# Optimization experiments

Hardware: AMD Instinct MI355X
Metric: run time of the kernel (lower is better)

Reference implementation:

```python
import jax, jax.numpy as jnp
import numpy as np

NEG = -9.0e15
EPS = 1e-5  # torch BatchNorm1d default eps


def _chain_idx(n):
    # chain graph with self loops; row-major nonzero ordering (matches torch .nonzero())
    rows, cols = [], []
    for i in range(n):
        for j in (i - 1, i, i + 1):
            if 0 <= j < n:
                rows.append(i); cols.append(j)
    return np.asarray(rows, np.int32), np.asarray(cols, np.int32)


def semgconv(x, W, e, rows, cols, n, b):
    # x: [B,N,Fin]; W: [2,Fin,Fout]; e: [nnz]; returns [B,N,Fout]
    h0 = jnp.einsum('bnf,fo->bno', x, W[0])
    h1 = jnp.einsum('bnf,fo->bno', x, W[1])
    logits = jnp.full((n, n), NEG, x.dtype).at[rows, cols].set(e)
    A = jax.nn.softmax(logits, axis=1)              # row-wise softmax over masked adjacency
    d = jnp.diagonal(A)                             # adj * I contribution
    A_off = A - jnp.diag(d)                         # adj * (1 - I)
    out = d[None, :, None] * h0 + jnp.einsum('ij,bjf->bif', A_off, h1)
    return out + b


def gblock(x, W, e, rows, cols, n, b, g, be):
    # SemGraphConv -> BatchNorm1d (training-mode batch stats over (B,N)) -> ReLU
    h = semgconv(x, W, e, rows, cols, n, b)
    mu = h.mean(axis=(0, 1))
    var = h.var(axis=(0, 1))
    h = g * (h - mu) * jax.lax.rsqrt(var + EPS) + be
    return jax.nn.relu(h)


def setup_inputs() -> dict:
    key = jax.random.key(0)
    ks = iter(jax.random.split(key, 40))
    B, NC, NS, H, HS = 4096, 32, 10, 160, 512  # HS = int(160/10*32)
    rc, cc = _chain_idx(NC)
    rs, cs = _chain_idx(NS)
    nnz_c, nnz_s = len(rc), len(rs)

    def w(shape, scale=0.1):
        return jax.random.normal(next(ks), shape, jnp.float32) * scale

    return dict(
        x_c=jax.random.normal(next(ks), (B, NC, 2), jnp.float32),
        x_s=jax.random.normal(next(ks), (B, NS, 2), jnp.float32),
        W_in=w((2, 2, H)), e_in=w((nnz_c,)) + 1.0, b_in=w((H,)),
        g_in=jnp.ones((H,), jnp.float32), be_in=jnp.zeros((H,), jnp.float32),
        W_s1=w((2, 2, HS)), e_s1=w((nnz_s,)) + 1.0, b_s1=w((HS,)),
        g_s1=jnp.ones((HS,), jnp.float32), be_s1=jnp.zeros((HS,), jnp.float32),
        W_c320=w((3, 2, 2 * H, H)), e_c320=w((3, nnz_c)) + 1.0, b_c320=w((3, H)),
        g_c320=jnp.ones((3, H), jnp.float32), be_c320=jnp.zeros((3, H), jnp.float32),
        W_c160=w((6, 2, H, H)), e_c160=w((6, nnz_c)) + 1.0, b_c160=w((6, H)),
        g_c160=jnp.ones((6, H), jnp.float32), be_c160=jnp.zeros((6, H), jnp.float32),
        W_s512=w((2, 2, HS, HS)), e_s512=w((2, nnz_s)) + 1.0, b_s512=w((2, HS)),
        g_s512=jnp.ones((2, HS), jnp.float32), be_s512=jnp.zeros((2, HS), jnp.float32),
        W_out=w((2, H, 2)), e_out=w((nnz_c,)) + 1.0, b_out=w((2,)),
        mc_r=jnp.asarray(rc), mc_c=jnp.asarray(cc),
        ms_r=jnp.asarray(rs), ms_c=jnp.asarray(cs),
    )


def reference(x_c, x_s, W_in, e_in, b_in, g_in, be_in,
              W_s1, e_s1, b_s1, g_s1, be_s1,
              W_c320, e_c320, b_c320, g_c320, be_c320,
              W_c160, e_c160, b_c160, g_c160, be_c160,
              W_s512, e_s512, b_s512, g_s512, be_s512,
              W_out, e_out, b_out, mc_r, mc_c, ms_r, ms_c):
    B, NC, NS, H = x_c.shape[0], 32, 10, 160
    c = gblock(x_c, W_in, e_in, mc_r, mc_c, NC, b_in, g_in, be_in)
    s = gblock(x_s, W_s1, e_s1, ms_r, ms_c, NS, b_s1, g_s1, be_s1)   # [B,10,512]
    for i in range(3):  # c_block1..3 interleaved with s_block2..3
        s_r = jnp.transpose(s, (0, 2, 1)).reshape(B, NC, H)          # [B,512,10] -> [B,32,160]
        c = gblock(jnp.concatenate([c, s_r], axis=2),
                   W_c320[i], e_c320[i], mc_r, mc_c, NC,
                   b_c320[i], g_c320[i], be_c320[i])
        h = gblock(c, W_c160[2 * i], e_c160[2 * i], mc_r, mc_c, NC,
                   b_c160[2 * i], g_c160[2 * i], be_c160[2 * i])
        h = gblock(h, W_c160[2 * i + 1], e_c160[2 * i + 1], mc_r, mc_c, NC,
                   b_c160[2 * i + 1], g_c160[2 * i + 1], be_c160[2 * i + 1])
        c = c + h                                                     # _ResGraphConv residual
        if i < 2:
            s = gblock(s, W_s512[i], e_s512[i], ms_r, ms_c, NS,
                       b_s512[i], g_s512[i], be_s512[i])
    return jax.nn.sigmoid(semgconv(c, W_out, e_out, mc_r, mc_c, NC, b_out))
```

## Files before the change

### kernel.cpp

```cpp
#include <hip/hip_runtime.h>
#include <hip/hip_bf16.h>

typedef __hip_bfloat16 bf16;
typedef unsigned short u16;
typedef __attribute__((ext_vector_type(8))) short short8;
typedef __attribute__((ext_vector_type(8))) unsigned short u16x8;
typedef __attribute__((ext_vector_type(4))) float f32x4;

#define B_SZ  4096
#define NCN   32
#define NSN   10
#define MC    (B_SZ*NCN)
#define MS    (B_SZ*NSN)
#define BUF_ELEMS 20971520UL

#define MODE_IN  0
#define MODE_PL  1
#define MODE_CC  2

#define DT_BF16  0
#define DT_F32   1
#define DT_PROBE 2

#define PART_SLOTS 163840
#define W_TOTAL    3411968

__device__ __forceinline__ float bf2f(bf16 v) { return __bfloat162float(v); }
__device__ __forceinline__ float ldv(const void* p, int dt, int idx) {
    return dt ? ((const float*)p)[idx] : bf2f(((const bf16*)p)[idx]);
}
__device__ __forceinline__ int resolve(int dt, const u16* probe) {
    return (dt == DT_PROBE) ? ((probe[0] == 0x3F80u) ? DT_BF16 : DT_F32) : dt;
}
__device__ __forceinline__ u16 f2bfbits(float f) {
    unsigned u = __builtin_bit_cast(unsigned, f);
    u += 0x7FFFu + ((u >> 16) & 1u);
    return (u16)(u >> 16);
}
__device__ __forceinline__ float bits2f(u16 u) {
    return __builtin_bit_cast(float, (unsigned)u << 16);
}
__device__ __forceinline__ void gload_lds16(const u16* g, u16* l) {
    __builtin_amdgcn_global_load_lds(
        (const __attribute__((address_space(1))) void*)g,
        (__attribute__((address_space(3))) void*)l, 16, 0, 0);
}
__device__ __forceinline__ size_t cfrag_addr(int r, int k) {
    int RT = r >> 8, within = r & 255;
    int g = ((within >> 6) << 2) | ((within >> 4) & 3);
    int tg = k >> 5, q = (k >> 3) & 3, j = k & 7;
    return ((((size_t)RT * 5 + tg) * 16 + g) * 64 + q * 16 + (r & 15)) * 8 + j;
}

struct WD { const void* src; int srcOff; int dstOff; int K; int F; };
struct WArgs { WD d[13]; };

__global__ void presplit_kernel(WArgs a, const u16* __restrict__ probe,
                                u16* __restrict__ Wf) {
    WD D = a.d[blockIdx.y];
    int nsteps = (D.K + 31) / 32;
    int total = (D.F / 32) * nsteps * 4096;
    int idx = blockIdx.x * blockDim.x + threadIdx.x;
    if (idx >= total) return;
    int dt = resolve(DT_PROBE, probe);
    int per = nsteps * 4096;
    int chunk = idx / per;  int rem = idx - chunk * per;
    int s = rem >> 12;      int slot = rem & 4095;
    int half = slot >> 11;  int sl = slot & 2047;
    int nt = sl >> 9;       int within = sl & 511;
    int lane = within >> 3; int j = within & 7;
    int q = lane >> 4, l15 = lane & 15;
    int plane = nt >> 1;
    int fcol = chunk * 32 + (nt & 1) * 16 + l15;
    int k = s * 32 + q * 8 + j;
    float v = (k < D.K) ? ldv(D.src, dt, D.srcOff + plane * D.K * D.F + k * D.F + fcol) : 0.f;
    u16 hb = f2bfbits(v);
    Wf[D.dstOff + idx] = half ? f2bfbits(v - bits2f(hb)) : hb;
}

struct CD { const void* e; int off; int n; };
struct CArgs { CD d[14]; };

__global__ void coeffs_all(CArgs a, const u16* __restrict__ probe, float* __restrict__ cfb) {
    CD D = a.d[blockIdx.x];
    float* cf = cfb + blockIdx.x * 96;
    int dt = resolve(DT_PROBE, probe);
    int i = threadIdx.x;
    if (i >= D.n) return;
    bool hasL = (i > 0), hasR = (i < D.n - 1);
    int off = D.off + ((i == 0) ? 0 : (3 * i - 1));
    float el = hasL ? ldv(D.e, dt, off) : 0.f;
    float es = ldv(D.e, dt, off + (hasL ? 1 : 0));
    float er = hasR ? ldv(D.e, dt, off + (hasL ? 2 : 1)) : 0.f;
    float m = es;
    if (hasL) m = fmaxf(m, el);
    if (hasR) m = fmaxf(m, er);
    float xl = hasL ? expf(el - m) : 0.f;
    float xs = expf(es - m);
    float xr = hasR ? expf(er - m) : 0.f;
    float inv = 1.f / (xl + xs + xr);
    cf[i]           = xl * inv;
    cf[D.n + i]     = xs * inv;
    cf[2 * D.n + i] = xr * inv;
}

template<int WAVES, int NODES, int KT, int TMODE, int AFRAG>
__global__ __launch_bounds__(WAVES * 64, (WAVES == 4) ? 4 : 3) void gemm_mfma(
    const u16* __restrict__ Wf, int wtOff,
    const u16* __restrict__ aHi, const u16* __restrict__ bHi2,
    const void* __restrict__ raw,
    const void* __restrict__ bias, int bOff,
    const u16* __restrict__ probe, const float* __restrict__ cf,
    u16* __restrict__ Thi,
    float* __restrict__ sumP, float* __restrict__ sqP, int F)
{
    constexpr int THREADS = WAVES * 64;
    constexpr int ROWS   = WAVES * 64;
    constexpr int nsteps = (KT + 31) / 32;
    constexpr int CHUNK  = (nsteps % 5 == 0) ? 5 : ((nsteps % 4 == 0) ? 4 : 1);
    constexpr int NCHUNK = nsteps / CHUNK;
    constexpr int NGRP   = WAVES * 4;
    constexpr int W_BYTES   = CHUNK * 8192;
    constexpr int VL_BYTES  = ROWS * 36 * 4;
    constexpr int RED_ONE   = 32 * (WAVES * 4) * 4;
    constexpr int EPI_BYTES = VL_BYTES + 2 * RED_ONE;
    constexpr int SMEM_SZ   = (W_BYTES > EPI_BYTES) ? W_BYTES : EPI_BYTES;

    const int tid  = threadIdx.x;
    const int wave = tid >> 6, lane = tid & 63;
    const int l15  = lane & 15, q = lane >> 4;

    const int NY   = F >> 5;
    const int nwg  = gridDim.x;
    const int NX   = nwg / NY;
    const int orig = blockIdx.x;
    const int xcd  = orig & 7, pos = orig >> 3;
    const int qch  = nwg >> 3, rch = nwg & 7;
    const int lin  = (xcd < rch ? xcd * (qch + 1)
                                : rch * (qch + 1) + (xcd - rch) * qch) + pos;
    const int bx   = lin / NY;
    const int by   = lin - bx * NY;
    const int f0   = by * 32;
    const int row0 = bx * ROWS;
    const int wdt  = resolve(DT_PROBE, probe);

    __shared__ __align__(16) char smem[SMEM_SZ];
    u16* Wt = (u16*)smem;
    float (*Vl)[36] = (float(*)[36])smem;
    float (*redS)[WAVES * 4] = (float(*)[WAVES * 4])(smem + VL_BYTES);
    float (*redQ)[WAVES * 4] = (float(*)[WAVES * 4])(smem + VL_BYTES + RED_ONE);

    const u16* wbase = Wf + wtOff + (size_t)by * nsteps * 4096;

    f32x4 acc[4][4];
#pragma unroll
    for (int a = 0; a < 4; ++a)
#pragma unroll
        for (int b = 0; b < 4; ++b) acc[a][b] = (f32x4){0.f, 0.f, 0.f, 0.f};

    if constexpr (TMODE == MODE_IN) {
        if (tid < 256) {
#pragma unroll
            for (int i = 0; i < 2; ++i) {
                int vs = i * 256 + tid;
                *(short8*)&Wt[vs * 8] = *(const short8*)(wbase + vs * 8);
            }
        }
        __syncthreads();
        short8 ahh[4], alo[4];
        const int kbase = q * 8;
#pragma unroll
        for (int mt = 0; mt < 4; ++mt) {
            int R = row0 + wave * 64 + mt * 16 + l15;
#pragma unroll
            for (int j = 0; j < 8; ++j) {
                int k = kbase + j;
                float v = (k < KT) ? ldv(raw, wdt, R * KT + k) : 0.f;
                u16 hb = f2bfbits(v);
                ahh[mt][j] = (short)hb;
                alo[mt][j] = (short)f2bfbits(v - bits2f(hb));
            }
        }
#pragma unroll
        for (int nt = 0; nt < 4; ++nt) {
            short8 bh = *(const short8*)&Wt[(nt * 64 + lane) * 8];
            short8 bl = *(const short8*)&Wt[2048 + (nt * 64 + lane) * 8];
#pragma unroll
            for (int mt = 0; mt < 4; ++mt) {
                acc[mt][nt] = __builtin_amdgcn_mfma_f32_16x16x32_bf16(ahh[mt], bh, acc[mt][nt], 0, 0, 0);
                acc[mt][nt] = __builtin_amdgcn_mfma_f32_16x16x32_bf16(ahh[mt], bl, acc[mt][nt], 0, 0, 0);
            }
#pragma unroll
            for (int mt = 0; mt < 4; ++mt)
                acc[mt][nt] = __builtin_amdgcn_mfma_f32_16x16x32_bf16(alo[mt], bh, acc[mt][nt], 0, 0, 0);
        }
        __syncthreads();
    } else {
        for (int c0 = 0; c0 < NCHUNK; ++c0) {
            {
                const u16* wc = wbase + (size_t)c0 * CHUNK * 4096;
                constexpr int SLOTS = CHUNK * 512;
#pragma unroll
                for (int base = 0; base < SLOTS; base += THREADS) {
                    int b2 = base + wave * 64;
                    if (b2 < SLOTS)
                        gload_lds16(wc + (size_t)(b2 + lane) * 8, Wt + (size_t)b2 * 8);
                }
            }
            __syncthreads();
#pragma unroll
            for (int sc = 0; sc < CHUNK; ++sc) {
                const int tg = c0 * CHUNK + sc;
                short8 ah[4];
                if constexpr (AFRAG == 1) {
#pragma unroll
                    for (int mt = 0; mt < 4; ++mt)
                        ah[mt] = *(const short8*)(aHi +
                            ((((size_t)bx * nsteps + tg) * NGRP) + (wave * 4 + mt)) * 512 + lane * 8);
                } else if constexpr (AFRAG == 3) {
                    const u16* base = (tg >= 5) ? bHi2 : aHi;
                    const int tgp = (tg >= 5) ? tg - 5 : tg;
#pragma unroll
                    for (int mt = 0; mt < 4; ++mt)
                        ah[mt] = *(const short8*)(base +
                            ((((size_t)bx * 5 + tgp) * 16) + (wave * 4 + mt)) * 512 + lane * 8);
                } else {
                    const int kbase = tg * 32 + q * 8;
                    const u16* hp; int stride, col;
                    if (TMODE == MODE_CC && kbase >= 160) { hp = bHi2; stride = 160; col = kbase - 160; }
                    else { hp = aHi; stride = (TMODE == MODE_CC) ? 160 : KT; col = kbase; }
#pragma unroll
                    for (int mt = 0; mt < 4; ++mt) {
                        size_t R = (size_t)(row0 + wave * 64 + mt * 16 + l15);
                        ah[mt] = *(const short8*)(hp + R * stride + col);
                    }
                }
#pragma unroll
                for (int nt = 0; nt < 4; ++nt) {
                    short8 bh = *(const short8*)&Wt[sc * 4096 + (nt * 64 + lane) * 8];
                    short8 bl = *(const short8*)&Wt[sc * 4096 + 2048 + (nt * 64 + lane) * 8];
#pragma unroll
                    for (int mt = 0; mt < 4; ++mt) {
                        acc[mt][nt] = __builtin_amdgcn_mfma_f32_16x16x32_bf16(ah[mt], bh, acc[mt][nt], 0, 0, 0);
                        acc[mt][nt] = __builtin_amdgcn_mfma_f32_16x16x32_bf16(ah[mt], bl, acc[mt][nt], 0, 0, 0);
                    }
                }
            }
            __syncthreads();
        }
    }

#pragma unroll
    for (int mt = 0; mt < 4; ++mt)
#pragma unroll
        for (int vt = 0; vt < 2; ++vt)
#pragma unroll
            for (int j = 0; j < 4; ++j)
                Vl[wave * 64 + mt * 16 + q * 4 + j][vt * 16 + l15] = acc[mt][2 + vt][j];
    __syncthreads();
    float bv0 = ldv(bias, wdt, bOff + f0 + l15);
    float bv1 = ldv(bias, wdt, bOff + f0 + 16 + l15);
    float cS[2] = {0.f, 0.f}, cQ[2] = {0.f, 0.f};
#pragma unroll
    for (int mt = 0; mt < 4; ++mt) {
#pragma unroll
        for (int j = 0; j < 4; ++j) {
            int r = wave * 64 + mt * 16 + q * 4 + j;
            int i = r % NODES;
            int rm = (i > 0)         ? r - 1 : r;
            int rp = (i < NODES - 1) ? r + 1 : r;
            float cl = cf[i], cs = cf[NODES + i], cr = cf[2 * NODES + i];
#pragma unroll
            for (int nt = 0; nt < 2; ++nt) {
                int c = nt * 16 + l15;
                float h = cs * acc[mt][nt][j] + cl * Vl[rm][c] + cr * Vl[rp][c]
                        + (nt ? bv1 : bv0);
                Thi[(size_t)(row0 + r) * F + f0 + c] = f2bfbits(h);
                cS[nt] += h; cQ[nt] += h * h;
            }
        }
    }
    redS[l15][wave * 4 + q] = cS[0];      redQ[l15][wave * 4 + q] = cQ[0];
    redS[16 + l15][wave * 4 + q] = cS[1]; redQ[16 + l15][wave * 4 + q] = cQ[1];
    __syncthreads();
    if (tid < 32) {
        float s = 0.f, t2 = 0.f;
#pragma unroll
        for (int t = 0; t < WAVES * 4; ++t) { s += redS[tid][t]; t2 += redQ[tid][t]; }
        sumP[(f0 + tid) * NX + bx] = s;
        sqP [(f0 + tid) * NX + bx] = t2;
    }
}

__global__ void bn_finalize(const float* __restrict__ sumP, const float* __restrict__ sqP,
                            int gridX, const void* __restrict__ g, int gOff,
                            const void* __restrict__ be, int beOff,
                            const u16* __restrict__ probe, float invM,
                            float* __restrict__ scale, float* __restrict__ shift) {
    int f = blockIdx.x;
    int t = threadIdx.x;
    __shared__ float ss[256], qq[256];
    float s = 0.f, q = 0.f;
    for (int i = t; i < gridX; i += 256) { s += sumP[f * gridX + i]; q += sqP[f * gridX + i]; }
    ss[t] = s; qq[t] = q;
    __syncthreads();
    for (int o = 128; o > 0; o >>= 1) {
        if (t < o) { ss[t] += ss[t + o]; qq[t] += qq[t + o]; }
        __syncthreads();
    }
    if (t == 0) {
        int dt = resolve(DT_PROBE, probe);
        float mu  = ss[0] * invM;
        float var = fmaf(-mu, mu, qq[0] * invM);
        float inv = rsqrtf(var + 1e-5f);
        float sc  = ldv(g, dt, gOff + f) * inv;
        scale[f] = sc;
        shift[f] = ldv(be, dt, beOff + f) - mu * sc;
    }
}

__global__ void bn_apply_frag(const u16* __restrict__ Thi,
                              const float* __restrict__ scale, const float* __restrict__ shift,
                              const u16* __restrict__ resHi,
                              u16* __restrict__ dst, int total8) {
    int slot = blockIdx.x * blockDim.x + threadIdx.x;
    if (slot >= total8) return;
    int lane = slot & 63; int rest = slot >> 6;
    int g = rest & 15;    int rs = rest >> 4;
    int s = rs % 5;       int RT = rs / 5;
    int l15 = lane & 15, q = lane >> 4;
    int row = RT * 256 + (g >> 2) * 64 + (g & 3) * 16 + l15;
    int col = s * 32 + q * 8;
    u16x8 th = *(const u16x8*)(Thi + (size_t)row * 160 + col);
    float v[8];
#pragma unroll
    for (int j = 0; j < 8; ++j)
        v[j] = fmaxf(fmaf(scale[col + j], bits2f(th[j]), shift[col + j]), 0.f);
    if (resHi) {
        u16x8 rh = *(const u16x8*)(resHi + (size_t)slot * 8);
#pragma unroll
        for (int j = 0; j < 8; ++j) v[j] += bits2f(rh[j]);
    }
    u16x8 oh;
#pragma unroll
    for (int j = 0; j < 8; ++j) oh[j] = f2bfbits(v[j]);
    *(u16x8*)(dst + (size_t)slot * 8) = oh;
}

__global__ __launch_bounds__(256) void bn_apply_s(
    const u16* __restrict__ Thi,
    const float* __restrict__ scale, const float* __restrict__ shift,
    u16* __restrict__ dstS, u16* __restrict__ dstR) {
    __shared__ u16 tile[10 * 520];
    const int t = threadIdx.x;
    const int b = blockIdx.x;
    const size_t baseT = (size_t)b * 5120;
#pragma unroll
    for (int i = 0; i < 3; ++i) {
        int slot = t + 256 * i;
        if (slot < 640) {
            int s0 = slot * 8;
            int qn = s0 >> 9, p0 = s0 & 511;
            u16x8 th = *(const u16x8*)(Thi + baseT + s0);
            u16x8 oh;
#pragma unroll
            for (int j = 0; j < 8; ++j)
                oh[j] = f2bfbits(fmaxf(fmaf(scale[p0 + j], bits2f(th[j]), shift[p0 + j]), 0.f));
            *(u16x8*)&tile[qn * 520 + p0] = oh;
            int within = (b & 31) * 10 + qn;
            int g = (within >> 6) * 4 + ((within >> 4) & 3);
            int l15 = within & 15;
            int tg = p0 >> 5, q = (p0 >> 3) & 3;
            size_t slotF = ((((size_t)(b >> 5) * 16 + tg) * 20) + g) * 64 + q * 16 + l15;
            *(u16x8*)(dstS + slotF * 8) = oh;
        }
    }
    __syncthreads();
#pragma unroll
    for (int i = 0; i < 3; ++i) {
        int slot = t + 256 * i;
        if (slot < 640) {
            int o0 = slot * 8;
            int rw = o0 / 160, cl0 = o0 - rw * 160;
            u16x8 oh;
#pragma unroll
            for (int j = 0; j < 8; ++j) {
                int o = o0 + j;
                int p = o / 10, qn = o - p * 10;
                oh[j] = tile[qn * 520 + p];
            }
            int within = (b & 7) * 32 + rw;
            int g = (within >> 6) * 4 + ((within >> 4) & 3);
            int l15 = within & 15;
            int tg = cl0 >> 5, q = (cl0 >> 3) & 3;
            size_t slotF = ((((size_t)(b >> 3) * 5 + tg) * 16) + g) * 64 + q * 16 + l15;
            *(u16x8*)(dstR + slotF * 8) = oh;
        }
    }
}

__global__ void out_kernel(const u16* __restrict__ cHi,
                           const void* __restrict__ W, const void* __restrict__ bias,
                           const float* __restrict__ cf,
                           const u16* __restrict__ probe,
                           void* __restrict__ out) {
    int gtid = blockIdx.x * blockDim.x + threadIdx.x;
    int r = gtid >> 6;
    int lane = gtid & 63;
    if (r >= MC) return;
    int wDt = resolve(DT_PROBE, probe);
    int i = r & 31;
    float cl = cf[i], cs = cf[32 + i], cr = cf[64 + i];
    int rm = (i > 0)  ? r - 1 : r;
    int rp = (i < 31) ? r + 1 : r;
    float ps0 = 0.f, ps1 = 0.f, pn0 = 0.f, pn1 = 0.f;
    for (int k = lane; k < 160; k += 64) {
        float xs = bits2f(cHi[cfrag_addr(r, k)]);
        float xn = cl * bits2f(cHi[cfrag_addr(rm, k)])
                 + cr * bits2f(cHi[cfrag_addr(rp, k)]);
        float w00 = ldv(W, wDt, k * 2),       w01 = ldv(W, wDt, k * 2 + 1);
        float w10 = ldv(W, wDt, 320 + k * 2), w11 = ldv(W, wDt, 320 + k * 2 + 1);
        ps0 = fmaf(xs, w00, ps0);
        ps1 = fmaf(xs, w01, ps1);
        pn0 = fmaf(xn, w10, pn0);
        pn1 = fmaf(xn, w11, pn1);
    }
#pragma unroll
    for (int off = 32; off > 0; off >>= 1) {
        ps0 += __shfl_down(ps0, off, 64);
        ps1 += __shfl_down(ps1, off, 64);
        pn0 += __shfl_down(pn0, off, 64);
        pn1 += __shfl_down(pn1, off, 64);
    }
    if (lane == 0) {
        float v0 = cs * ps0 + pn0 + ldv(bias, wDt, 0);
        float v1 = cs * ps1 + pn1 + ldv(bias, wDt, 1);
        float s0 = 1.f / (1.f + expf(-v0));
        float s1 = 1.f / (1.f + expf(-v1));
        if (probe[0] == 0x3F80u) {
            ((bf16*)out)[r * 2 + 0] = __float2bfloat16(s0);
            ((bf16*)out)[r * 2 + 1] = __float2bfloat16(s1);
        } else {
            ((float*)out)[r * 2 + 0] = s0;
            ((float*)out)[r * 2 + 1] = s1;
        }
    }
}

extern "C" void kernel_launch(void* const* d_in, const int* in_sizes, int n_in,
                              void* d_out, int out_size, void* d_ws, size_t ws_size,
                              hipStream_t stream) {
    const u16* probe = (const u16*)d_in[5];

    float* sumP  = (float*)d_ws;
    float* sqP   = sumP + PART_SLOTS;
    float* scale = sqP + PART_SLOTS;
    float* shift = scale + 512;
    float* cfb   = shift + 512;
    u16*   Wf    = (u16*)(cfb + 14 * 96);
    char*  p     = (char*)(Wf + W_TOTAL);

    size_t PL = 2 * BUF_ELEMS;
    u16 *Thi = (u16*)p; p += PL;
    u16 *Chi = (u16*)p; p += PL;
    u16 *Shi = (u16*)p; p += PL;
    u16 *Hhi = (u16*)p; p += PL;
    (void)ws_size;

    WArgs wa;
    int wo = 0; int di = 0;
    auto addW = [&](const void* src, int sOff, int K, int F) {
        wa.d[di++] = WD{src, sOff, wo, K, F};
        wo += (F / 32) * ((K + 31) / 32) * 4096;
    };
    addW(d_in[2], 0, 2, 160);
    addW(d_in[7], 0, 2, 512);
    for (int i = 0; i < 3; ++i) addW(d_in[12], i * 102400, 320, 160);
    for (int i = 0; i < 6; ++i) addW(d_in[17], i * 51200, 160, 160);
    for (int i = 0; i < 2; ++i) addW(d_in[22], i * 524288, 512, 512);
    presplit_kernel<<<dim3(4096, 13), 256, 0, stream>>>(wa, probe, Wf);

    CArgs ca;
    int ci = 0;
    auto addC = [&](const void* e, int off, int n) { ca.d[ci++] = CD{e, off, n}; };
    addC(d_in[3], 0, 32);
    addC(d_in[8], 0, 10);
    for (int i = 0; i < 3; ++i) addC(d_in[13], i * 94, 32);
    for (int i = 0; i < 6; ++i) addC(d_in[18], i * 94, 32);
    for (int i = 0; i < 2; ++i) addC(d_in[23], i * 28, 10);
    addC(d_in[28], 0, 32);
    coeffs_all<<<14, 64, 0, stream>>>(ca, probe, cfb);

    const int wtIn = 0, wtS1 = 20480, wtC320 = 86016, wtC160 = 700416, wtS512 = 1314816;

    auto post_c = [&](const void* g, int gOff, const void* be, int beOff,
                      u16* dHi, const u16* rHi) {
        bn_finalize<<<160, 256, 0, stream>>>(sumP, sqP, 512, g, gOff, be, beOff,
                                             probe, 1.f / (float)MC, scale, shift);
        bn_apply_frag<<<MC * 160 / 8 / 256, 256, 0, stream>>>(
            Thi, scale, shift, rHi, dHi, MC * 160 / 8);
    };
    auto post_s = [&](const void* g, int gOff, const void* be, int beOff) {
        bn_finalize<<<512, 256, 0, stream>>>(sumP, sqP, 128, g, gOff, be, beOff,
                                             probe, 1.f / (float)MS, scale, shift);
        bn_apply_s<<<B_SZ, 256, 0, stream>>>(Thi, scale, shift, Shi, Hhi);
    };

    const dim3 gc(512 * 5), gs(128 * 16);

    gemm_mfma<4, 32, 2, MODE_IN, 0><<<gc, 256, 0, stream>>>(
        Wf, wtIn, nullptr, nullptr, d_in[0], d_in[4], 0, probe, cfb + 0 * 96,
        Thi, sumP, sqP, 160);
    post_c(d_in[5], 0, d_in[6], 0, Chi, nullptr);

    gemm_mfma<5, 10, 2, MODE_IN, 0><<<gs, 320, 0, stream>>>(
        Wf, wtS1, nullptr, nullptr, d_in[1], d_in[9], 0, probe, cfb + 1 * 96,
        Thi, sumP, sqP, 512);
    post_s(d_in[10], 0, d_in[11], 0);

    for (int i = 0; i < 3; ++i) {
        gemm_mfma<4, 32, 320, MODE_CC, 3><<<gc, 256, 0, stream>>>(
            Wf, wtC320 + i * 204800, Chi, Hhi, nullptr, d_in[14], i * 160,
            probe, cfb + (2 + i) * 96, Thi, sumP, sqP, 160);
        post_c(d_in[15], i * 160, d_in[16], i * 160, Chi, nullptr);

        gemm_mfma<4, 32, 160, MODE_PL, 1><<<gc, 256, 0, stream>>>(
            Wf, wtC160 + (2 * i) * 102400, Chi, nullptr, nullptr, d_in[19], (2 * i) * 160,
            probe, cfb + (5 + 2 * i) * 96, Thi, sumP, sqP, 160);
        post_c(d_in[20], (2 * i) * 160, d_in[21], (2 * i) * 160, Hhi, nullptr);

        gemm_mfma<4, 32, 160, MODE_PL, 1><<<gc, 256, 0, stream>>>(
            Wf, wtC160 + (2 * i + 1) * 102400, Hhi, nullptr, nullptr, d_in[19], (2 * i + 1) * 160,
            probe, cfb + (6 + 2 * i) * 96, Thi, sumP, sqP, 160);
        post_c(d_in[20], (2 * i + 1) * 160, d_in[21], (2 * i + 1) * 160, Chi, Chi);

        if (i < 2) {
            gemm_mfma<5, 10, 512, MODE_PL, 1><<<gs, 320, 0, stream>>>(
                Wf, wtS512 + i * 1048576, Shi, nullptr, nullptr, d_in[24], i * 512,
                probe, cfb + (11 + i) * 96, Thi, sumP, sqP, 512);
            post_s(d_in[25], i * 512, d_in[26], i * 512);
        }
    }

    out_kernel<<<(MC * 64 + 255) / 256, 256, 0, stream>>>(Chi, d_in[27], d_in[29],
                                                          cfb + 13 * 96, probe, d_out);
}
```

Baseline: 1.205 ms.

## Shrink GEMM LDS footprint: smaller weight chunks, plain loads, split epilogue staging

Cuts the weight staging chunk from up to five K-steps to two, replaces direct global-to-LDS loads with plain vector loads through registers done by the first 256 threads, and stages the epilogue neighbor values in two 16-column passes instead of one 32-column pass. Together these shrink shared memory per block, presumably to let more workgroups reside per CU. In exchange there are more barrier round trips over the K loop and in the epilogue. Register-routed weight loads may also raise VGPR pressure and lose the async LDS-load path.

```diff
diff --git a/kernel.cpp b/kernel.cpp
--- a/kernel.cpp
+++ b/kernel.cpp
@@ -39,11 +39,6 @@
 }
 __device__ __forceinline__ float bits2f(u16 u) {
     return __builtin_bit_cast(float, (unsigned)u << 16);
-}
-__device__ __forceinline__ void gload_lds16(const u16* g, u16* l) {
-    __builtin_amdgcn_global_load_lds(
-        (const __attribute__((address_space(1))) void*)g,
-        (__attribute__((address_space(3))) void*)l, 16, 0, 0);
 }
 __device__ __forceinline__ size_t cfrag_addr(int r, int k) {
     int RT = r >> 8, within = r & 255;
@@ -114,14 +109,13 @@
     u16* __restrict__ Thi,
     float* __restrict__ sumP, float* __restrict__ sqP, int F)
 {
-    constexpr int THREADS = WAVES * 64;
     constexpr int ROWS   = WAVES * 64;
     constexpr int nsteps = (KT + 31) / 32;
-    constexpr int CHUNK  = (nsteps % 5 == 0) ? 5 : ((nsteps % 4 == 0) ? 4 : 1);
+    constexpr int CHUNK  = (nsteps % 2 == 0) ? 2 : 1;
     constexpr int NCHUNK = nsteps / CHUNK;
     constexpr int NGRP   = WAVES * 4;
     constexpr int W_BYTES   = CHUNK * 8192;
-    constexpr int VL_BYTES  = ROWS * 36 * 4;
+    constexpr int VL_BYTES  = ROWS * 18 * 4;
     constexpr int RED_ONE   = 32 * (WAVES * 4) * 4;
     constexpr int EPI_BYTES = VL_BYTES + 2 * RED_ONE;
     constexpr int SMEM_SZ   = (W_BYTES > EPI_BYTES) ? W_BYTES : EPI_BYTES;
@@ -146,7 +140,7 @@
 
     __shared__ __align__(16) char smem[SMEM_SZ];
     u16* Wt = (u16*)smem;
-    float (*Vl)[36] = (float(*)[36])smem;
+    float (*Vl)[18] = (float(*)[18])smem;
     float (*redS)[WAVES * 4] = (float(*)[WAVES * 4])(smem + VL_BYTES);
     float (*redQ)[WAVES * 4] = (float(*)[WAVES * 4])(smem + VL_BYTES + RED_ONE);
 
@@ -197,14 +191,12 @@
         __syncthreads();
     } else {
         for (int c0 = 0; c0 < NCHUNK; ++c0) {
-            {
+            if (tid < 256) {
                 const u16* wc = wbase + (size_t)c0 * CHUNK * 4096;
-                constexpr int SLOTS = CHUNK * 512;
-#pragma unroll
-                for (int base = 0; base < SLOTS; base += THREADS) {
-                    int b2 = base + wave * 64;
-                    if (b2 < SLOTS)
-                        gload_lds16(wc + (size_t)(b2 + lane) * 8, Wt + (size_t)b2 * 8);
+#pragma unroll
+                for (int i = 0; i < CHUNK * 2; ++i) {
+                    int vs = i * 256 + tid;
+                    *(short8*)&Wt[vs * 8] = *(const short8*)(wc + vs * 8);
                 }
             }
             __syncthreads();
@@ -250,36 +242,35 @@
         }
     }
 
-#pragma unroll
-    for (int mt = 0; mt < 4; ++mt)
-#pragma unroll
-        for (int vt = 0; vt < 2; ++vt)
-#pragma unroll
-            for (int j = 0; j < 4; ++j)
-                Vl[wave * 64 + mt * 16 + q * 4 + j][vt * 16 + l15] = acc[mt][2 + vt][j];
-    __syncthreads();
     float bv0 = ldv(bias, wdt, bOff + f0 + l15);
     float bv1 = ldv(bias, wdt, bOff + f0 + 16 + l15);
     float cS[2] = {0.f, 0.f}, cQ[2] = {0.f, 0.f};
 #pragma unroll
-    for (int mt = 0; mt < 4; ++mt) {
-#pragma unroll
-        for (int j = 0; j < 4; ++j) {
-            int r = wave * 64 + mt * 16 + q * 4 + j;
-            int i = r % NODES;
-            int rm = (i > 0)         ? r - 1 : r;
-            int rp = (i < NODES - 1) ? r + 1 : r;
-            float cl = cf[i], cs = cf[NODES + i], cr = cf[2 * NODES + i];
-#pragma unroll
-            for (int nt = 0; nt < 2; ++nt) {
-                int c = nt * 16 + l15;
-                float h = cs * acc[mt][nt][j] + cl * Vl[rm][c] + cr * Vl[rp][c]
-                        + (nt ? bv1 : bv0);
-                Thi[(size_t)(row0 + r) * F + f0 + c] = f2bfbits(h);
-                cS[nt] += h; cQ[nt] += h * h;
-            }
-        }
-    }
+    for (int vt = 0; vt < 2; ++vt) {
+        if (vt) __syncthreads();
+#pragma unroll
+        for (int mt = 0; mt < 4; ++mt)
+#pragma unroll
+            for (int j = 0; j < 4; ++j)
+                Vl[wave * 64 + mt * 16 + q * 4 + j][l15] = acc[mt][2 + vt][j];
+        __syncthreads();
+#pragma unroll
+        for (int mt = 0; mt < 4; ++mt) {
+#pragma unroll
+            for (int j = 0; j < 4; ++j) {
+                int r = wave * 64 + mt * 16 + q * 4 + j;
+                int i = r % NODES;
+                int rm = (i > 0)         ? r - 1 : r;
+                int rp = (i < NODES - 1) ? r + 1 : r;
+                float cl = cf[i], cs = cf[NODES + i], cr = cf[2 * NODES + i];
+                float h = cs * acc[mt][vt][j] + cl * Vl[rm][l15] + cr * Vl[rp][l15]
+                        + (vt ? bv1 : bv0);
+                Thi[(size_t)(row0 + r) * F + f0 + vt * 16 + l15] = f2bfbits(h);
+                cS[vt] += h; cQ[vt] += h * h;
+            }
+        }
+    }
+    __syncthreads();
     redS[l15][wave * 4 + q] = cS[0];      redQ[l15][wave * 4 + q] = cQ[0];
     redS[16 + l15][wave * 4 + q] = cS[1]; redQ[16 + l15][wave * 4 + q] = cQ[1];
     __syncthreads();
```

After: 1.287 ms. 1.07x slower.
